# Optimization experiments

Measured on AMD Instinct MI355X. Metric: run time of the kernel, lower is better.

The kernel has to match this reference:

```python
import jax, jax.numpy as jnp
import numpy as np

B, S, NX, NH = 4, 1024, 1024, 16
HD = NX // NH  # 64


def setup_inputs() -> dict:
    key = jax.random.key(0)
    k1, k2, k3 = jax.random.split(key, 3)
    return {
        "hidden_states": jax.random.normal(k1, (B, S, NX), dtype=jnp.float32),
        "c_attn_w": jax.random.normal(k2, (NX, 3 * NX), dtype=jnp.float32) * 0.02,
        "c_attn_b": jnp.zeros((3 * NX,), dtype=jnp.float32),
        "c_proj_w": jax.random.normal(k3, (NX, NX), dtype=jnp.float32) * 0.02,
        "c_proj_b": jnp.zeros((NX,), dtype=jnp.float32),
    }


def reference(hidden_states, c_attn_w, c_attn_b, c_proj_w, c_proj_b):
    # Conv1D fused QKV projection: x @ W + b, then split into q,k,v
    qkv = hidden_states @ c_attn_w + c_attn_b  # [B,S,3*NX]
    q, k, v = jnp.split(qkv, 3, axis=-1)
    # split heads -> [B, H, S, D]
    def heads(x):
        return x.reshape(B, S, NH, HD).transpose(0, 2, 1, 3)
    q, k, v = heads(q), heads(k), heads(v)
    # scores: q @ k^T / sqrt(D)  (scale=True; NOTE: no causal mask in this fork)
    w = jnp.einsum("bhqd,bhkd->bhqk", q, k) / jnp.sqrt(jnp.asarray(HD, q.dtype))
    w = jax.nn.softmax(w, axis=-1)
    a = jnp.einsum("bhqk,bhkd->bhqd", w, v)  # [B,H,S,D]
    # merge heads -> [B,S,NX]
    a = a.transpose(0, 2, 1, 3).reshape(B, S, NX)
    # output projection (dropout is identity in eval)
    return a @ c_proj_w + c_proj_b
```

## Files before the change

kernel.cpp:

```cpp
#include <hip/hip_runtime.h>
#include <hip/hip_fp16.h>
#include <cmath>

constexpr int Bb  = 4;
constexpr int Ss  = 1024;
constexpr int NXc = 1024;
constexpr int NHc = 16;
constexpr int HDc = 64;

typedef __bf16    bf16x8 __attribute__((ext_vector_type(8)));
typedef _Float16  f16x8  __attribute__((ext_vector_type(8)));
typedef float     f32x4  __attribute__((ext_vector_type(4)));
typedef unsigned short ushortT;
typedef ushortT ushort8v __attribute__((ext_vector_type(8)));
typedef unsigned uint2v  __attribute__((ext_vector_type(2)));

#define QSCALE 0.18033688011112042f

__device__ __forceinline__ ushortT f2h_bits(float x) {
  return __half_as_ushort(__float2half(x));
}

__device__ __forceinline__ void gll16(const void* g, void* l) {
  __builtin_amdgcn_global_load_lds(
      (const __attribute__((address_space(1))) unsigned int*)g,
      (__attribute__((address_space(3))) unsigned int*)l, 16, 0, 0);
}

__device__ __forceinline__ void drain_vmem() {
  asm volatile("s_waitcnt vmcnt(0)" ::: "memory");
  __builtin_amdgcn_sched_barrier(0);
}

__global__ __launch_bounds__(256) void prep_all(
    const float* __restrict__ hs, const float* __restrict__ aw,
    const float* __restrict__ pw,
    ushortT* __restrict__ hF, ushortT* __restrict__ awT,
    ushortT* __restrict__ pwT)
{
  const int bid = blockIdx.x;
  if (bid < 4096) {
    int i = (bid * 256 + threadIdx.x) * 4;
    float4 v = *reinterpret_cast<const float4*>(&hs[i]);
    *reinterpret_cast<ushort4*>(&hF[i]) =
        make_ushort4(f2h_bits(v.x), f2h_bits(v.y), f2h_bits(v.z), f2h_bits(v.w));
    return;
  }
  __shared__ float tile[32][33];
  const int tx = threadIdx.x & 31, ty = threadIdx.x >> 5;
  if (bid < 7168) {
    const int b2 = bid - 4096;
    const int n0 = (b2 % 96) * 32, k0 = (b2 / 96) * 32;
    #pragma unroll
    for (int i = 0; i < 4; ++i)
      tile[ty + i * 8][tx] = aw[(size_t)(k0 + ty + i * 8) * 3072 + n0 + tx];
    __syncthreads();
    #pragma unroll
    for (int i = 0; i < 4; ++i)
      awT[(size_t)(n0 + ty + i * 8) * 1024 + k0 + tx] = f2h_bits(tile[tx][ty + i * 8]);
  } else {
    const int b2 = bid - 7168;
    const int n0 = (b2 & 31) * 32, k0 = (b2 >> 5) * 32;
    #pragma unroll
    for (int i = 0; i < 4; ++i)
      tile[ty + i * 8][tx] = pw[(size_t)(k0 + ty + i * 8) * 1024 + n0 + tx];
    __syncthreads();
    #pragma unroll
    for (int i = 0; i < 4; ++i)
      pwT[(size_t)(n0 + ty + i * 8) * 1024 + k0 + tx] = f2h_bits(tile[tx][ty + i * 8]);
  }
}

__global__ __launch_bounds__(256) void gemm_f16_qkv(
    const ushortT* __restrict__ A16, const ushortT* __restrict__ B16,
    const float* __restrict__ bias,
    ushortT* __restrict__ Qb, ushortT* __restrict__ Kb,
    ushortT* __restrict__ Vt, int M, int N, int K)
{
  constexpr int BK = 64;
  __shared__ ushortT smem[32768];

  const int t    = threadIdx.x;
  const int lane = t & 63;
  const int w    = t >> 6;
  const int wr   = w >> 1, wc = w & 1;
  const int lin = blockIdx.y * 24 + blockIdx.x;
  const int swz = (lin & 7) * 96 + (lin >> 3);
  const int m0 = (swz / 24) * 128;
  const int n0 = (swz % 24) * 128;
  const int l15 = lane & 15;
  const int g   = lane >> 4;

  const int srow  = w * 32 + (lane >> 3);
  const int sslot = (lane & 7) ^ (lane >> 3);

  f32x4 acc[4][4];
  #pragma unroll
  for (int m = 0; m < 4; ++m)
    #pragma unroll
    for (int n = 0; n < 4; ++n)
      #pragma unroll
      for (int r = 0; r < 4; ++r) acc[m][n][r] = 0.f;

  const ushortT* pA = A16 + (size_t)(m0 + srow) * K + sslot * 8;
  const ushortT* pB = B16 + (size_t)(n0 + srow) * K + sslot * 8;

  auto STAGE = [&](ushortT* buf, int k0) {
    #pragma unroll
    for (int i = 0; i < 4; ++i) {
      const size_t gstep = (size_t)i * 8 * K + k0;
      const int    loff  = (w * 32 + i * 8) * BK;
      gll16(pA + gstep, &buf[loff]);
      gll16(pB + gstep, &buf[8192 + loff]);
    }
  };

  const int arow = wr * 64 + l15;
  const int bcol = wc * 64 + l15;

  auto COMPUTE = [&](const ushortT* buf) {
    const ushortT* sA = buf;
    const ushortT* sB = buf + 8192;
    #pragma unroll
    for (int c = 0; c < 2; ++c) {
      const int slot = c * 4 + g;
      f16x8 af[4], bf[4];
      #pragma unroll
      for (int m = 0; m < 4; ++m) {
        int r   = arow + m * 16;
        int off = r * BK + ((slot ^ (r & 7)) * 8);
        af[m] = *reinterpret_cast<const f16x8*>(&sA[off]);
      }
      #pragma unroll
      for (int n = 0; n < 4; ++n) {
        int r   = bcol + n * 16;
        int off = r * BK + ((slot ^ (r & 7)) * 8);
        bf[n] = *reinterpret_cast<const f16x8*>(&sB[off]);
      }
      #pragma unroll
      for (int m = 0; m < 4; ++m)
        #pragma unroll
        for (int n = 0; n < 4; ++n)
          acc[m][n] = __builtin_amdgcn_mfma_f32_16x16x32_f16(af[m], bf[n], acc[m][n], 0, 0, 0);
    }
  };

  const int nt = K / BK;
  STAGE(&smem[0], 0);
  drain_vmem();
  __syncthreads();
  for (int tt = 0; tt < nt; tt += 2) {
    if (tt + 1 < nt) STAGE(&smem[16384], (tt + 1) * BK);
    COMPUTE(&smem[0]);
    drain_vmem();
    __syncthreads();
    if (tt + 2 < nt) STAGE(&smem[0], (tt + 2) * BK);
    COMPUTE(&smem[16384]);
    drain_vmem();
    __syncthreads();
  }

  const int region = n0 >> 10;
  if (region < 2) {
    #pragma unroll
    for (int n = 0; n < 4; ++n) {
      int col_g = n0 + wc * 64 + n * 16 + l15;
      int colm  = col_g & 1023;
      float bv  = bias[col_g];
      #pragma unroll
      for (int m = 0; m < 4; ++m) {
        int row = m0 + wr * 64 + m * 16 + (g << 2);
        #pragma unroll
        for (int r = 0; r < 4; ++r) {
          float v = acc[m][n][r] + bv;
          if (region == 0)
            Qb[(size_t)(row + r) * 1024 + colm] = f2h_bits(v * QSCALE);
          else
            Kb[(size_t)(row + r) * 1024 + colm] = f2h_bits(v);
        }
      }
    }
  } else {
    ushortT* T = smem;
    #pragma unroll
    for (int n = 0; n < 4; ++n) {
      int cl   = wc * 64 + n * 16 + l15;
      float bv = bias[n0 + cl];
      #pragma unroll
      for (int m = 0; m < 4; ++m) {
        int rl = wr * 64 + m * 16 + (g << 2);
        #pragma unroll
        for (int r = 0; r < 4; ++r)
          T[cl * 136 + rl + r] = f2h_bits(acc[m][n][r] + bv);
      }
    }
    __syncthreads();
    const int c  = t >> 1;
    const int rh = (t & 1) * 64;
    const int nn = (n0 - 2048) + c;
    const int hh = nn >> 6, dd = nn & 63;
    const int bb = m0 >> 10;
    const int sl = (m0 & 1023) + rh;
    size_t vbase = ((size_t)((bb * 16 + hh) * 64 + dd)) * 1024 + sl;
    #pragma unroll
    for (int j = 0; j < 8; ++j) {
      ushort8v v = *reinterpret_cast<const ushort8v*>(&T[c * 136 + rh + j * 8]);
      *reinterpret_cast<ushort8v*>(&Vt[vbase + j * 8]) = v;
    }
  }
}

__global__ __launch_bounds__(256) void gemm_f16s(
    const ushortT* __restrict__ A16, const ushortT* __restrict__ B16,
    const float* __restrict__ bias, float* __restrict__ C,
    int M, int N, int K)
{
  constexpr int BK = 64;
  __shared__ ushortT smem[32768];

  const int t    = threadIdx.x;
  const int lane = t & 63;
  const int w    = t >> 6;
  const int wr   = w >> 1, wc = w & 1;
  const int lin = blockIdx.y * 8 + blockIdx.x;
  const int swz = (lin & 7) * 32 + (lin >> 3);
  const int m0 = (swz / 8) * 128;
  const int n0 = (swz % 8) * 128;
  const int l15 = lane & 15;
  const int g   = lane >> 4;

  const int srow  = w * 32 + (lane >> 3);
  const int sslot = (lane & 7) ^ (lane >> 3);

  f32x4 acc[4][4];
  #pragma unroll
  for (int m = 0; m < 4; ++m)
    #pragma unroll
    for (int n = 0; n < 4; ++n)
      #pragma unroll
      for (int r = 0; r < 4; ++r) acc[m][n][r] = 0.f;

  const ushortT* pA = A16 + (size_t)(m0 + srow) * K + sslot * 8;
  const ushortT* pB = B16 + (size_t)(n0 + srow) * K + sslot * 8;

  auto STAGE = [&](ushortT* buf, int k0) {
    #pragma unroll
    for (int i = 0; i < 4; ++i) {
      const size_t gstep = (size_t)i * 8 * K + k0;
      const int    loff  = (w * 32 + i * 8) * BK;
      gll16(pA + gstep, &buf[loff]);
      gll16(pB + gstep, &buf[8192 + loff]);
    }
  };

  const int arow = wr * 64 + l15;
  const int bcol = wc * 64 + l15;

  auto COMPUTE = [&](const ushortT* buf) {
    const ushortT* sA = buf;
    const ushortT* sB = buf + 8192;
    #pragma unroll
    for (int c = 0; c < 2; ++c) {
      const int slot = c * 4 + g;
      f16x8 af[4], bf[4];
      #pragma unroll
      for (int m = 0; m < 4; ++m) {
        int r   = arow + m * 16;
        int off = r * BK + ((slot ^ (r & 7)) * 8);
        af[m] = *reinterpret_cast<const f16x8*>(&sA[off]);
      }
      #pragma unroll
      for (int n = 0; n < 4; ++n) {
        int r   = bcol + n * 16;
        int off = r * BK + ((slot ^ (r & 7)) * 8);
        bf[n] = *reinterpret_cast<const f16x8*>(&sB[off]);
      }
      #pragma unroll
      for (int m = 0; m < 4; ++m)
        #pragma unroll
        for (int n = 0; n < 4; ++n)
          acc[m][n] = __builtin_amdgcn_mfma_f32_16x16x32_f16(af[m], bf[n], acc[m][n], 0, 0, 0);
    }
  };

  const int nt = K / BK;
  STAGE(&smem[0], 0);
  drain_vmem();
  __syncthreads();
  for (int tt = 0; tt < nt; tt += 2) {
    if (tt + 1 < nt) STAGE(&smem[16384], (tt + 1) * BK);
    COMPUTE(&smem[0]);
    drain_vmem();
    __syncthreads();
    if (tt + 2 < nt) STAGE(&smem[0], (tt + 2) * BK);
    COMPUTE(&smem[16384]);
    drain_vmem();
    __syncthreads();
  }

  #pragma unroll
  for (int n = 0; n < 4; ++n) {
    int col  = n0 + wc * 64 + n * 16 + l15;
    float bv = bias[col];
    #pragma unroll
    for (int m = 0; m < 4; ++m) {
      int row = m0 + wr * 64 + m * 16 + (g << 2);
      #pragma unroll
      for (int r = 0; r < 4; ++r)
        C[(size_t)(row + r) * N + col] = acc[m][n][r] + bv;
    }
  }
}

__global__ __launch_bounds__(256) void attn_mfma(
    const ushortT* __restrict__ Qb, const ushortT* __restrict__ Kb,
    const ushortT* __restrict__ Vt, ushortT* __restrict__ xF)
{
  __shared__ ushortT sK[64 * 64];
  __shared__ ushortT sV[64 * 64];
  __shared__ ushortT sP[64 * 64];

  const int t    = threadIdx.x;
  const int lane = t & 63;
  const int w    = t >> 6;
  const int bh = blockIdx.x, b = bh >> 4, h = bh & 15;
  const int q0 = blockIdx.y * 64;
  const int l15 = lane & 15;
  const int g   = lane >> 4;

  f16x8 qa[2];
  #pragma unroll
  for (int ks = 0; ks < 2; ++ks) {
    size_t addr = (size_t)(b * 1024 + q0 + w * 16 + l15) * 1024
                  + h * 64 + ks * 32 + g * 8;
    qa[ks] = *reinterpret_cast<const f16x8*>(&Qb[addr]);
  }

  f16x8 ones;
  #pragma unroll
  for (int j = 0; j < 8; ++j) ones[j] = (_Float16)1.0f;

  const int srow  = lane >> 3;
  const int sslot = (lane & 7) ^ srow;

  f32x4 O[4];
  f32x4 lO;
  #pragma unroll
  for (int r = 0; r < 4; ++r) lO[r] = 0.f;
  #pragma unroll
  for (int n = 0; n < 4; ++n)
    #pragma unroll
    for (int r = 0; r < 4; ++r) O[n][r] = 0.f;

  const int prow  = w * 16 + l15;
  const int pbase = prow * 64 + (g & 1) * 4;
  const int pcs0  = g >> 1;

  for (int kt = 0; kt < 16; ++kt) {
    const int k0 = kt * 64;
    #pragma unroll
    for (int i = 0; i < 2; ++i) {
      int r = w * 16 + i * 8 + srow;
      gll16(&Kb[(size_t)(b * 1024 + k0 + r) * 1024 + h * 64 + sslot * 8],
            &sK[(w * 16 + i * 8) * 64]);
      gll16(&Vt[((size_t)bh * 64 + r) * 1024 + k0 + sslot * 8],
            &sV[(w * 16 + i * 8) * 64]);
    }
    __syncthreads();

    f32x4 st[4];
    #pragma unroll
    for (int n = 0; n < 4; ++n)
      #pragma unroll
      for (int r = 0; r < 4; ++r) st[n][r] = 0.f;

    #pragma unroll
    for (int ks = 0; ks < 2; ++ks) {
      f16x8 kb[4];
      #pragma unroll
      for (int n = 0; n < 4; ++n) {
        int row = n * 16 + l15;
        kb[n] = *reinterpret_cast<const f16x8*>(
            &sK[row * 64 + (((g + ks * 4) ^ (row & 7)) * 8)]);
      }
      #pragma unroll
      for (int n = 0; n < 4; ++n)
        st[n] = __builtin_amdgcn_mfma_f32_16x16x32_f16(kb[n], qa[ks], st[n], 0, 0, 0);
    }

    #pragma unroll
    for (int n = 0; n < 4; ++n) {
      ushortT p4[4];
      #pragma unroll
      for (int r = 0; r < 4; ++r)
        p4[r] = f2h_bits(exp2f(st[n][r]));
      uint2v pk;
      pk.x = (unsigned)p4[0] | ((unsigned)p4[1] << 16);
      pk.y = (unsigned)p4[2] | ((unsigned)p4[3] << 16);
      int cs = n * 2 + pcs0;
      *reinterpret_cast<uint2v*>(&sP[pbase + ((cs ^ (prow & 7)) << 3)]) = pk;
    }

    #pragma unroll
    for (int ks = 0; ks < 2; ++ks) {
      f16x8 vb[4], pa;
      #pragma unroll
      for (int n = 0; n < 4; ++n) {
        int rd = n * 16 + l15;
        vb[n] = *reinterpret_cast<const f16x8*>(
            &sV[rd * 64 + (((g + ks * 4) ^ (rd & 7)) * 8)]);
      }
      {
        int pr = w * 16 + l15;
        pa = *reinterpret_cast<const f16x8*>(
            &sP[pr * 64 + (((g + ks * 4) ^ (pr & 7)) * 8)]);
      }
      #pragma unroll
      for (int n = 0; n < 4; ++n)
        O[n] = __builtin_amdgcn_mfma_f32_16x16x32_f16(pa, vb[n], O[n], 0, 0, 0);
      lO = __builtin_amdgcn_mfma_f32_16x16x32_f16(pa, ones, lO, 0, 0, 0);
    }
    __syncthreads();
  }

  #pragma unroll
  for (int r = 0; r < 4; ++r) {
    float inv = 1.f / lO[r];
    #pragma unroll
    for (int n = 0; n < 4; ++n) {
      size_t off = (size_t)(b * 1024 + q0 + w * 16 + g * 4 + r) * 1024
                   + h * 64 + n * 16 + l15;
      xF[off] = f2h_bits(O[n][r] * inv);
    }
  }
}

extern "C" void kernel_launch(void* const* d_in, const int* in_sizes, int n_in,
                              void* d_out, int out_size, void* d_ws, size_t ws_size,
                              hipStream_t stream) {
  const float* hs = (const float*)d_in[0];
  const float* aw = (const float*)d_in[1];
  const float* ab = (const float*)d_in[2];
  const float* pw = (const float*)d_in[3];
  const float* pb = (const float*)d_in[4];
  float* out = (float*)d_out;

  char* ws = (char*)d_ws;
  const int M = Bb * Ss;

  ushortT* hF  = (ushortT*)(ws);
  ushortT* awT = (ushortT*)(ws + ( 8u << 20));
  ushortT* pwT = (ushortT*)(ws + (14u << 20));
  ushortT* Qb  = (ushortT*)(ws + (18u << 20));
  ushortT* Kb  = (ushortT*)(ws + (26u << 20));
  ushortT* Vt  = (ushortT*)(ws + (34u << 20));
  ushortT* xF  = (ushortT*)(ws + (42u << 20));

  dim3 blk(256);

  prep_all<<<8192, blk, 0, stream>>>(hs, aw, pw, hF, awT, pwT);
  gemm_f16_qkv<<<dim3(24, 32), blk, 0, stream>>>(
      hF, awT, ab, Qb, Kb, Vt, M, 3 * NXc, NXc);
  attn_mfma<<<dim3(Bb * NHc, Ss / 64), blk, 0, stream>>>(Qb, Kb, Vt, xF);
  gemm_f16s<<<dim3(8, 32), blk, 0, stream>>>(
      xF, pwT, pb, out, M, NXc, NXc);
}
```

Measured before the change: 97.69 us.

## Double attention key tile to 128 and alias P buffer onto K shared memory

The attention kernel now processes 128 keys per iteration instead of 64, halving loop trips and block barriers over the sequence. The P (probability) tile reuses the K shared buffer after an extra barrier, which keeps LDS footprint similar while the V tile grows to 64x128. It adds an explicit vmem drain and a third barrier per iteration. Register pressure also rises from eight score accumulators, which may affect occupancy.

Measured after the change: 100.6 us. 3.0% more time.

```diff
diff --git a/kernel.cpp b/kernel.cpp
--- a/kernel.cpp
+++ b/kernel.cpp
@@ -316,9 +316,8 @@
     const ushortT* __restrict__ Qb, const ushortT* __restrict__ Kb,
     const ushortT* __restrict__ Vt, ushortT* __restrict__ xF)
 {
-  __shared__ ushortT sK[64 * 64];
-  __shared__ ushortT sV[64 * 64];
-  __shared__ ushortT sP[64 * 64];
+  __shared__ ushortT sKP[128 * 64];
+  __shared__ ushortT sV[64 * 128];
 
   const int t    = threadIdx.x;
   const int lane = t & 63;
@@ -340,8 +339,10 @@
   #pragma unroll
   for (int j = 0; j < 8; ++j) ones[j] = (_Float16)1.0f;
 
-  const int srow  = lane >> 3;
-  const int sslot = (lane & 7) ^ srow;
+  const int srowK  = lane >> 3;
+  const int sslotK = (lane & 7) ^ srowK;
+  const int srowV = lane >> 4;
+  const int pV    = lane & 15;
 
   f32x4 O[4];
   f32x4 lO;
@@ -352,44 +353,52 @@
     #pragma unroll
     for (int r = 0; r < 4; ++r) O[n][r] = 0.f;
 
-  const int prow  = w * 16 + l15;
-  const int pbase = prow * 64 + (g & 1) * 4;
-  const int pcs0  = g >> 1;
-
-  for (int kt = 0; kt < 16; ++kt) {
-    const int k0 = kt * 64;
-    #pragma unroll
-    for (int i = 0; i < 2; ++i) {
-      int r = w * 16 + i * 8 + srow;
-      gll16(&Kb[(size_t)(b * 1024 + k0 + r) * 1024 + h * 64 + sslot * 8],
-            &sK[(w * 16 + i * 8) * 64]);
-      gll16(&Vt[((size_t)bh * 64 + r) * 1024 + k0 + sslot * 8],
-            &sV[(w * 16 + i * 8) * 64]);
-    }
-    __syncthreads();
-
-    f32x4 st[4];
-    #pragma unroll
-    for (int n = 0; n < 4; ++n)
+  const int prow = w * 16 + l15;
+  const int pkey = prow & 7;
+  const int psub = (g & 1) * 4;
+  const int pg2  = g >> 1;
+
+  for (int kt = 0; kt < 8; ++kt) {
+    const int k0 = kt * 128;
+    #pragma unroll
+    for (int i = 0; i < 4; ++i) {
+      int r = w * 32 + i * 8 + srowK;
+      gll16(&Kb[(size_t)(b * 1024 + k0 + r) * 1024 + h * 64 + sslotK * 8],
+            &sKP[(w * 32 + i * 8) * 64]);
+    }
+    #pragma unroll
+    for (int i = 0; i < 4; ++i) {
+      int row = w * 16 + i * 4 + srowV;
+      int pc  = pV ^ (row & 7);
+      gll16(&Vt[((size_t)bh * 64 + row) * 1024 + k0 + pc * 8],
+            &sV[(w * 16 + i * 4) * 128]);
+    }
+    drain_vmem();
+    __syncthreads();
+
+    f32x4 st[8];
+    #pragma unroll
+    for (int n = 0; n < 8; ++n)
       #pragma unroll
       for (int r = 0; r < 4; ++r) st[n][r] = 0.f;
 
     #pragma unroll
     for (int ks = 0; ks < 2; ++ks) {
-      f16x8 kb[4];
-      #pragma unroll
-      for (int n = 0; n < 4; ++n) {
+      f16x8 kb[8];
+      #pragma unroll
+      for (int n = 0; n < 8; ++n) {
         int row = n * 16 + l15;
         kb[n] = *reinterpret_cast<const f16x8*>(
-            &sK[row * 64 + (((g + ks * 4) ^ (row & 7)) * 8)]);
-      }
-      #pragma unroll
-      for (int n = 0; n < 4; ++n)
+            &sKP[row * 64 + (((g + ks * 4) ^ (row & 7)) * 8)]);
+      }
+      #pragma unroll
+      for (int n = 0; n < 8; ++n)
         st[n] = __builtin_amdgcn_mfma_f32_16x16x32_f16(kb[n], qa[ks], st[n], 0, 0, 0);
     }
-
-    #pragma unroll
-    for (int n = 0; n < 4; ++n) {
+    __syncthreads();
+
+    #pragma unroll
+    for (int n = 0; n < 8; ++n) {
       ushortT p4[4];
       #pragma unroll
       for (int r = 0; r < 4; ++r)
@@ -397,24 +406,22 @@
       uint2v pk;
       pk.x = (unsigned)p4[0] | ((unsigned)p4[1] << 16);
       pk.y = (unsigned)p4[2] | ((unsigned)p4[3] << 16);
-      int cs = n * 2 + pcs0;
-      *reinterpret_cast<uint2v*>(&sP[pbase + ((cs ^ (prow & 7)) << 3)]) = pk;
-    }
-
-    #pragma unroll
-    for (int ks = 0; ks < 2; ++ks) {
+      int cs = n * 2 + pg2;
+      *reinterpret_cast<uint2v*>(
+          &sKP[prow * 128 + ((cs ^ pkey) << 3) + psub]) = pk;
+    }
+
+    #pragma unroll
+    for (int ks = 0; ks < 4; ++ks) {
       f16x8 vb[4], pa;
       #pragma unroll
       for (int n = 0; n < 4; ++n) {
         int rd = n * 16 + l15;
         vb[n] = *reinterpret_cast<const f16x8*>(
-            &sV[rd * 64 + (((g + ks * 4) ^ (rd & 7)) * 8)]);
-      }
-      {
-        int pr = w * 16 + l15;
-        pa = *reinterpret_cast<const f16x8*>(
-            &sP[pr * 64 + (((g + ks * 4) ^ (pr & 7)) * 8)]);
-      }
+            &sV[rd * 128 + (((ks * 4 + g) ^ (rd & 7)) * 8)]);
+      }
+      pa = *reinterpret_cast<const f16x8*>(
+          &sKP[prow * 128 + (((ks * 4 + g) ^ pkey) * 8)]);
       #pragma unroll
       for (int n = 0; n < 4; ++n)
         O[n] = __builtin_amdgcn_mfma_f32_16x16x32_f16(pa, vb[n], O[n], 0, 0, 0);
```
